# Kernel tuning notes

Measured on AMD Instinct MI355X. Metric: run time of the kernel, lower is better.

The kernel has to match this reference:

```python
import jax, jax.numpy as jnp
import numpy as np

B, S, T, D = 64, 256, 8, 256
E, M = 500000, 2048
NEG_INF = -10000000000.0


def setup_inputs() -> dict:
    key = jax.random.key(0)
    ks = jax.random.split(key, 9)
    token_reprs = jax.random.normal(ks[0], (B, S, T, D), dtype=jnp.float32)
    w1 = jax.random.normal(ks[1], (D, D // 2), dtype=jnp.float32) * (1.0 / np.sqrt(D))
    b1 = jnp.zeros((D // 2,), dtype=jnp.float32)
    w2 = jax.random.normal(ks[2], (D // 2, 1), dtype=jnp.float32) * (1.0 / np.sqrt(D // 2))
    b2 = jnp.zeros((1,), dtype=jnp.float32)
    edge_index = jax.random.randint(ks[3], (2, E), 0, B * S, dtype=jnp.int32)
    lm_indices = jax.random.randint(ks[4], (M,), 0, B * S * T, dtype=jnp.int32)
    batch_pointers = jax.random.randint(ks[5], (M,), 0, B, dtype=jnp.int32)
    tree_padding_mask = jax.random.randint(ks[6], (B, S), 0, 2, dtype=jnp.int32).astype(jnp.bool_)
    return {
        "token_reprs": token_reprs,
        "w1": w1, "b1": b1, "w2": w2, "b2": b2,
        "edge_index": edge_index,
        "lm_indices": lm_indices,
        "batch_pointers": batch_pointers,
        "tree_padding_mask": tree_padding_mask,
    }


def reference(token_reprs, w1, b1, w2, b2, edge_index, lm_indices, batch_pointers, tree_padding_mask):
    b, s, t, d = token_reprs.shape
    # type representation is the first token of each type tree
    type_reprs = token_reprs[:, :, 0]                  # [B, S, D]
    flat_types = type_reprs.reshape(b * s, d)          # [B*S, D]

    # predict_lemmas: gather scope/goal reprs, elementwise multiply, 2-layer MLP
    scope_ids, goal_ids = edge_index[0], edge_index[1]
    h = flat_types[scope_ids] * flat_types[goal_ids]   # [E, D]
    h = h @ w1 + b1                                    # [E, D//2] (Dropout is identity in eval)
    lemmas = (h @ w2 + b2)[:, 0]                       # [E]

    # predict_masks: gather masked token reprs + per-tree candidates, dot, mask
    mask_reprs = token_reprs.reshape(b * s * t, d)[lm_indices]  # [M, D]
    candidates = type_reprs[batch_pointers]            # [M, S, D]
    candidate_mask = tree_padding_mask[batch_pointers] # [M, S]
    lm_preds = jnp.einsum('md,msd->ms', mask_reprs, candidates)
    lm_preds = jnp.where(candidate_mask, lm_preds, NEG_INF)
    return lemmas, lm_preds
```

## Files before the change

### kernel.cpp

```cpp
#include <hip/hip_runtime.h>

#define DD 256
#define SS 256
#define BB 64
#define NEDGE 500000
#define MM 2048
#define NEG_INF -10000000000.0f
#define ROWF4 512
#define NROWS (BB * SS)

#define OFF_VC     0
#define OFF_MSORT  4096
#define OFF_BSTART (4096 + MM * 4)
#define OFF_FSLAB  (1 << 16)
#define OFF_P2     ((1 << 16) + (4 << 20))
#define OFF_MROWS  ((1 << 16) + (12 << 20))

typedef float vf4 __attribute__((ext_vector_type(4)));
typedef float f32x2 __attribute__((ext_vector_type(2)));

__device__ __forceinline__ float bflo(unsigned u) { return __uint_as_float(u << 16); }
__device__ __forceinline__ float bfhi(unsigned u) { return __uint_as_float(u & 0xFFFF0000u); }
__device__ __forceinline__ unsigned short bf_rne(float f) {
    unsigned u = __float_as_uint(f);
    return (unsigned short)((u + 0x7FFFu + ((u >> 16) & 1u)) >> 16);
}
__device__ __forceinline__ unsigned pack2_rne(float a, float b) {
    return (unsigned)bf_rne(a) | ((unsigned)bf_rne(b) << 16);
}

#if __has_builtin(__builtin_amdgcn_cvt_pk_fp8_f32) && __has_builtin(__builtin_amdgcn_cvt_pk_f32_fp8)
#define FP8_HW 1
#else
#define FP8_HW 0
#endif

__device__ __forceinline__ unsigned char sw_f32_to_e4m3(float f) {
    unsigned u = __float_as_uint(f);
    unsigned s = (u >> 24) & 0x80u;
    float af = fabsf(f);
    if (af >= 448.f) return (unsigned char)(s | 0x7E);
    if (af < 0.015625f) {
        int q = (int)(af * 512.f + 0.5f);
        return (unsigned char)(s | (unsigned)q);
    }
    unsigned lsb = (u >> 20) & 1u;
    u += 0x7FFFFu + lsb;
    int e = (int)(u >> 23) - 120;
    unsigned m = (u >> 20) & 7u;
    if (e >= 16) return (unsigned char)(s | 0x7E);
    return (unsigned char)(s | ((unsigned)e << 3) | m);
}
__device__ __forceinline__ float sw_e4m3_to_f32(unsigned b) {
    unsigned s = (b & 0x80u) << 24;
    unsigned e = (b >> 3) & 0xFu, m = b & 7u;
    if (e == 0) {
        float v = (float)m * 0.001953125f;
        return (b & 0x80u) ? -v : v;
    }
    return __uint_as_float(s | ((e + 120u) << 23) | (m << 20));
}

__device__ __forceinline__ unsigned enc_fp8x4(float x, float y, float z, float w) {
#if FP8_HW
    int r = 0;
    r = __builtin_amdgcn_cvt_pk_fp8_f32(x, y, r, false);
    r = __builtin_amdgcn_cvt_pk_fp8_f32(z, w, r, true);
    return (unsigned)r;
#else
    return (unsigned)sw_f32_to_e4m3(x) | ((unsigned)sw_f32_to_e4m3(y) << 8)
         | ((unsigned)sw_f32_to_e4m3(z) << 16) | ((unsigned)sw_f32_to_e4m3(w) << 24);
#endif
}

__device__ __forceinline__ float dot4_fp8(unsigned aw, unsigned bw, const float4 v) {
#if FP8_HW
    f32x2 al = __builtin_amdgcn_cvt_pk_f32_fp8((int)aw, false);
    f32x2 ah = __builtin_amdgcn_cvt_pk_f32_fp8((int)aw, true);
    f32x2 bl = __builtin_amdgcn_cvt_pk_f32_fp8((int)bw, false);
    f32x2 bh = __builtin_amdgcn_cvt_pk_f32_fp8((int)bw, true);
    return (al.x * bl.x) * v.x + (al.y * bl.y) * v.y
         + (ah.x * bh.x) * v.z + (ah.y * bh.y) * v.w;
#else
    return sw_e4m3_to_f32(aw & 255u) * sw_e4m3_to_f32(bw & 255u) * v.x
         + sw_e4m3_to_f32((aw >> 8) & 255u) * sw_e4m3_to_f32((bw >> 8) & 255u) * v.y
         + sw_e4m3_to_f32((aw >> 16) & 255u) * sw_e4m3_to_f32((bw >> 16) & 255u) * v.z
         + sw_e4m3_to_f32(aw >> 24) * sw_e4m3_to_f32(bw >> 24) * v.w;
#endif
}

__global__ void setup_k(const float* __restrict__ w1, const float* __restrict__ b1,
                        const float* __restrict__ w2, const float* __restrict__ b2,
                        const int* __restrict__ bp,
                        float* __restrict__ vc, int* __restrict__ msorted,
                        int* __restrict__ bstart) {
    const int t = threadIdx.x;
    if (blockIdx.x == 0) {
        __shared__ float sw2[DD / 2];
        if (t < DD / 2) sw2[t] = w2[t];
        __syncthreads();
        const int lane = t & 63, w = t >> 6;
        for (int r = w; r < DD; r += 4) {
            float x = w1[r * (DD / 2) + lane] * sw2[lane]
                    + w1[r * (DD / 2) + 64 + lane] * sw2[64 + lane];
            x += __shfl_down(x, 32);
            x += __shfl_down(x, 16);
            x += __shfl_down(x, 8);
            x += __shfl_down(x, 4);
            x += __shfl_down(x, 2);
            x += __shfl_down(x, 1);
            if (lane == 0) vc[r] = x;
        }
        if (w == 0) {
            float x = b1[lane] * sw2[lane] + b1[64 + lane] * sw2[64 + lane];
            x += __shfl_down(x, 32);
            x += __shfl_down(x, 16);
            x += __shfl_down(x, 8);
            x += __shfl_down(x, 4);
            x += __shfl_down(x, 2);
            x += __shfl_down(x, 1);
            if (lane == 0) vc[DD] = x + b2[0];
        }
    } else {
        __shared__ int hist[BB];
        __shared__ int offs[BB + 1];
        if (t < BB) hist[t] = 0;
        __syncthreads();
        for (int m = t; m < MM; m += 256) atomicAdd(&hist[bp[m]], 1);
        __syncthreads();
        if (t == 0) {
            int acc = 0;
            for (int i = 0; i < BB; ++i) { offs[i] = acc; acc += hist[i]; }
            offs[BB] = acc;
        }
        __syncthreads();
        if (t < BB + 1) bstart[t] = offs[t];
        __syncthreads();
        for (int m = t; m < MM; m += 256) {
            int pos = atomicAdd(&offs[bp[m]], 1);
            msorted[pos] = m;
        }
    }
}

__global__ __launch_bounds__(256) void compact(
        const float* __restrict__ tok, const int* __restrict__ lmi,
        unsigned* __restrict__ fslab,
        unsigned* __restrict__ p2, unsigned* __restrict__ mrows) {
    const int lane = threadIdx.x & 63;
    const int w    = threadIdx.x >> 6;
    if (blockIdx.x < NROWS / 4) {
        const int row = blockIdx.x * 4 + w;
        const float4 a = ((const float4*)tok)[(size_t)row * ROWF4 + lane];
        fslab[(size_t)row * 64 + lane] = enc_fp8x4(a.x, a.y, a.z, a.w);
        const size_t pi = (size_t)row * 128 + lane * 2;
        p2[pi]     = pack2_rne(a.x, a.y);
        p2[pi + 1] = pack2_rne(a.z, a.w);
    } else {
        const int m = (blockIdx.x - NROWS / 4) * 4 + w;
        const float4 a = ((const float4*)(tok + (size_t)lmi[m] * DD))[lane];
        mrows[(size_t)m * 128 + lane * 2]     = pack2_rne(a.x, a.y);
        mrows[(size_t)m * 128 + lane * 2 + 1] = pack2_rne(a.z, a.w);
    }
}

__global__ __launch_bounds__(256) void edge_fp8(
        const unsigned* __restrict__ fslab,
        const int* __restrict__ edges, const float* __restrict__ vc,
        float* __restrict__ out) {
    const int t = threadIdx.x;
    const int lane = t & 63, w = t >> 6;
    const int l16 = lane & 15;
    const int g = lane >> 4;
    const int e0 = blockIdx.x * 256;

    __shared__ int sIdx[2][256];
    __shared__ float accs[256];
    const int e = e0 + t;
    const bool val = e < NEDGE;
    sIdx[0][t] = val ? __builtin_nontemporal_load(edges + e) : 0;
    sIdx[1][t] = val ? __builtin_nontemporal_load(edges + NEDGE + e) : 0;

    const float4 v0 = ((const float4*)vc)[l16 * 4 + 0];
    const float4 v1 = ((const float4*)vc)[l16 * 4 + 1];
    const float4 v2 = ((const float4*)vc)[l16 * 4 + 2];
    const float4 v3 = ((const float4*)vc)[l16 * 4 + 3];
    __syncthreads();

    #pragma unroll 4
    for (int it = 0; it < 16; ++it) {
        const int slot = w * 64 + it * 4 + g;
        const int sc = sIdx[0][slot];
        const int gl = sIdx[1][slot];
        const uint4 A = *(const uint4*)(fslab + (size_t)sc * 64 + l16 * 4);
        const uint4 B = *(const uint4*)(fslab + (size_t)gl * 64 + l16 * 4);
        float s = dot4_fp8(A.x, B.x, v0) + dot4_fp8(A.y, B.y, v1)
                + dot4_fp8(A.z, B.z, v2) + dot4_fp8(A.w, B.w, v3);
        s += __shfl_down(s, 8, 16);
        s += __shfl_down(s, 4, 16);
        s += __shfl_down(s, 2, 16);
        s += __shfl_down(s, 1, 16);
        if (l16 == 0) accs[slot] = s;
    }
    __syncthreads();
    const float c = vc[DD];
    if (val) __builtin_nontemporal_store(accs[t] + c, out + e);
}

__global__ __launch_bounds__(256) void lm_gemm(
        const unsigned* __restrict__ p2,
        const unsigned* __restrict__ mrows,
        const int* __restrict__ msorted,
        const int* __restrict__ bstart,
        const int* __restrict__ tpm,
        float* __restrict__ out) {
    const int b  = blockIdx.x;
    const int st = blockIdx.y;
    const int ch = blockIdx.z;
    const int s0 = bstart[b], s1 = bstart[b + 1];
    const int base = s0 + ch * 32;
    if (base >= s1) return;
    const int nm = min(32, s1 - base);
    const int t = threadIdx.x;

    __shared__ unsigned lmaskU[32 * 132];
    __shared__ unsigned srowU[32 * 132];
    __shared__ int mids[32];
    __shared__ int sact[64];
    __shared__ int snact;

    if (t < 32) mids[t] = msorted[base + min(t, nm - 1)];
    if (t >= 64 && t < 128) {
        int lt = t - 64;
        bool act = tpm[b * SS + st * 64 + lt] != 0;
        unsigned long long mk = __ballot(act);
        if (act) sact[__popcll(mk & ((1ull << lt) - 1))] = lt;
        if (lt == 0) snact = (int)__popcll(mk);
    }
    __syncthreads();

    for (int f = t; f < nm * 32; f += 256) {
        int r = f >> 5, q = f & 31;
        *(uint4*)&lmaskU[r * 132 + q * 4] = ((const uint4*)mrows)[(size_t)mids[r] * 32 + q];
    }
    for (int f = t; f < nm * 64; f += 256) {
        int i = f >> 6, c = f & 63;
        if (!tpm[b * SS + st * 64 + c])
            out[(size_t)mids[i] * SS + st * 64 + c] = NEG_INF;
    }
    __syncthreads();

    const int nact = snact;
    const int i2 = t & 15, sg = t >> 4;

    for (int g = 0; g * 32 < nact; ++g) {
        if (g) __syncthreads();
        const int nv = min(32, nact - g * 32);
        for (int f = t; f < nv * 32; f += 256) {
            int r = f >> 5, q = f & 31;
            size_t row = (size_t)b * SS + st * 64 + sact[g * 32 + r];
            *(uint4*)&srowU[r * 132 + q * 4] = ((const uint4*)p2)[row * 32 + q];
        }
        __syncthreads();

        float a00 = 0.f, a01 = 0.f, a10 = 0.f, a11 = 0.f;
        #pragma unroll 4
        for (int stp = 0; stp < 32; ++stp) {
            const uint4 A0 = *(const uint4*)&lmaskU[i2 * 132 + stp * 4];
            const uint4 A1 = *(const uint4*)&lmaskU[(i2 + 16) * 132 + stp * 4];
            const uint4 B0 = *(const uint4*)&srowU[sg * 132 + stp * 4];
            const uint4 B1 = *(const uint4*)&srowU[(sg + 16) * 132 + stp * 4];
            float a0[8], a1[8], b0[8], b1[8];
            a0[0] = bflo(A0.x); a0[1] = bfhi(A0.x); a0[2] = bflo(A0.y); a0[3] = bfhi(A0.y);
            a0[4] = bflo(A0.z); a0[5] = bfhi(A0.z); a0[6] = bflo(A0.w); a0[7] = bfhi(A0.w);
            a1[0] = bflo(A1.x); a1[1] = bfhi(A1.x); a1[2] = bflo(A1.y); a1[3] = bfhi(A1.y);
            a1[4] = bflo(A1.z); a1[5] = bfhi(A1.z); a1[6] = bflo(A1.w); a1[7] = bfhi(A1.w);
            b0[0] = bflo(B0.x); b0[1] = bfhi(B0.x); b0[2] = bflo(B0.y); b0[3] = bfhi(B0.y);
            b0[4] = bflo(B0.z); b0[5] = bfhi(B0.z); b0[6] = bflo(B0.w); b0[7] = bfhi(B0.w);
            b1[0] = bflo(B1.x); b1[1] = bfhi(B1.x); b1[2] = bflo(B1.y); b1[3] = bfhi(B1.y);
            b1[4] = bflo(B1.z); b1[5] = bfhi(B1.z); b1[6] = bflo(B1.w); b1[7] = bfhi(B1.w);
            #pragma unroll
            for (int jj = 0; jj < 8; ++jj) {
                a00 = fmaf(a0[jj], b0[jj], a00);
                a01 = fmaf(a0[jj], b1[jj], a01);
                a10 = fmaf(a1[jj], b0[jj], a10);
                a11 = fmaf(a1[jj], b1[jj], a11);
            }
        }

        const int iA = g * 32 + sg, iB = iA + 16;
        if (i2 < nm) {
            size_t ob = (size_t)mids[i2] * SS + st * 64;
            if (iA < nact) out[ob + sact[iA]] = a00;
            if (iB < nact) out[ob + sact[iB]] = a01;
        }
        if (i2 + 16 < nm) {
            size_t ob = (size_t)mids[i2 + 16] * SS + st * 64;
            if (iA < nact) out[ob + sact[iA]] = a10;
            if (iB < nact) out[ob + sact[iB]] = a11;
        }
    }
}

extern "C" void kernel_launch(void* const* d_in, const int* in_sizes, int n_in,
                              void* d_out, int out_size, void* d_ws, size_t ws_size,
                              hipStream_t stream) {
    const float* tok = (const float*)d_in[0];
    const float* w1  = (const float*)d_in[1];
    const float* b1  = (const float*)d_in[2];
    const float* w2  = (const float*)d_in[3];
    const float* b2  = (const float*)d_in[4];
    const int* edges = (const int*)d_in[5];
    const int* lmi   = (const int*)d_in[6];
    const int* bp    = (const int*)d_in[7];
    const int* tpm   = (const int*)d_in[8];

    float* out_lemmas = (float*)d_out;
    float* out_lm     = (float*)d_out + NEDGE;

    char* ws = (char*)d_ws;
    float* vc        = (float*)(ws + OFF_VC);
    int* msorted     = (int*)(ws + OFF_MSORT);
    int* bstart      = (int*)(ws + OFF_BSTART);
    unsigned* fslab  = (unsigned*)(ws + OFF_FSLAB);
    unsigned* p2     = (unsigned*)(ws + OFF_P2);
    unsigned* mrows  = (unsigned*)(ws + OFF_MROWS);

    setup_k<<<2, 256, 0, stream>>>(w1, b1, w2, b2, bp, vc, msorted, bstart);
    compact<<<NROWS / 4 + MM / 4, 256, 0, stream>>>(tok, lmi, fslab, p2, mrows);
    edge_fp8<<<(NEDGE + 255) / 256, 256, 0, stream>>>(fslab, edges, vc, out_lemmas);
    lm_gemm<<<dim3(BB, 4, 8), 256, 0, stream>>>(p2, mrows, msorted, bstart, tpm, out_lm);
}
```

Before: 261.4 us.

## Use bf16 MFMA in lm_gemm and merge setup and compact kernels

The scalar bf16-unpack FMA loop in lm_gemm is replaced with __builtin_amdgcn_mfma_f32_16x16x32_bf16, where each wave computes one 16x16 output tile, and the output indexing is remapped to match. The setup and compact kernels are merged into one prep kernel, saving a launch and letting the small setup work run alongside the compaction blocks. The MFMA path depends on getting the fragment layout exactly right. The bulk of the time is likely in compaction and the edge kernel, so the overall effect may be limited.

```diff
diff --git a/kernel.cpp b/kernel.cpp
--- a/kernel.cpp
+++ b/kernel.cpp
@@ -18,6 +18,8 @@
 
 typedef float vf4 __attribute__((ext_vector_type(4)));
 typedef float f32x2 __attribute__((ext_vector_type(2)));
+typedef float f32x4 __attribute__((ext_vector_type(4)));
+typedef short bf16x8 __attribute__((ext_vector_type(8)));
 
 __device__ __forceinline__ float bflo(unsigned u) { return __uint_as_float(u << 16); }
 __device__ __forceinline__ float bfhi(unsigned u) { return __uint_as_float(u & 0xFFFF0000u); }
@@ -89,17 +91,34 @@
 #endif
 }
 
-__global__ void setup_k(const float* __restrict__ w1, const float* __restrict__ b1,
-                        const float* __restrict__ w2, const float* __restrict__ b2,
-                        const int* __restrict__ bp,
-                        float* __restrict__ vc, int* __restrict__ msorted,
-                        int* __restrict__ bstart) {
+__global__ __launch_bounds__(256) void prep(
+        const float* __restrict__ tok, const int* __restrict__ lmi,
+        const float* __restrict__ w1, const float* __restrict__ b1,
+        const float* __restrict__ w2, const float* __restrict__ b2,
+        const int* __restrict__ bp,
+        unsigned* __restrict__ fslab,
+        unsigned* __restrict__ p2, unsigned* __restrict__ mrows,
+        float* __restrict__ vc, int* __restrict__ msorted,
+        int* __restrict__ bstart) {
     const int t = threadIdx.x;
-    if (blockIdx.x == 0) {
+    const int lane = t & 63;
+    const int w    = t >> 6;
+    if (blockIdx.x < NROWS / 4) {
+        const int row = blockIdx.x * 4 + w;
+        const float4 a = ((const float4*)tok)[(size_t)row * ROWF4 + lane];
+        fslab[(size_t)row * 64 + lane] = enc_fp8x4(a.x, a.y, a.z, a.w);
+        const size_t pi = (size_t)row * 128 + lane * 2;
+        p2[pi]     = pack2_rne(a.x, a.y);
+        p2[pi + 1] = pack2_rne(a.z, a.w);
+    } else if (blockIdx.x < NROWS / 4 + MM / 4) {
+        const int m = (blockIdx.x - NROWS / 4) * 4 + w;
+        const float4 a = ((const float4*)(tok + (size_t)lmi[m] * DD))[lane];
+        mrows[(size_t)m * 128 + lane * 2]     = pack2_rne(a.x, a.y);
+        mrows[(size_t)m * 128 + lane * 2 + 1] = pack2_rne(a.z, a.w);
+    } else if (blockIdx.x == NROWS / 4 + MM / 4) {
         __shared__ float sw2[DD / 2];
         if (t < DD / 2) sw2[t] = w2[t];
         __syncthreads();
-        const int lane = t & 63, w = t >> 6;
         for (int r = w; r < DD; r += 4) {
             float x = w1[r * (DD / 2) + lane] * sw2[lane]
                     + w1[r * (DD / 2) + 64 + lane] * sw2[64 + lane];
@@ -140,27 +159,6 @@
             int pos = atomicAdd(&offs[bp[m]], 1);
             msorted[pos] = m;
         }
-    }
-}
-
-__global__ __launch_bounds__(256) void compact(
-        const float* __restrict__ tok, const int* __restrict__ lmi,
-        unsigned* __restrict__ fslab,
-        unsigned* __restrict__ p2, unsigned* __restrict__ mrows) {
-    const int lane = threadIdx.x & 63;
-    const int w    = threadIdx.x >> 6;
-    if (blockIdx.x < NROWS / 4) {
-        const int row = blockIdx.x * 4 + w;
-        const float4 a = ((const float4*)tok)[(size_t)row * ROWF4 + lane];
-        fslab[(size_t)row * 64 + lane] = enc_fp8x4(a.x, a.y, a.z, a.w);
-        const size_t pi = (size_t)row * 128 + lane * 2;
-        p2[pi]     = pack2_rne(a.x, a.y);
-        p2[pi + 1] = pack2_rne(a.z, a.w);
-    } else {
-        const int m = (blockIdx.x - NROWS / 4) * 4 + w;
-        const float4 a = ((const float4*)(tok + (size_t)lmi[m] * DD))[lane];
-        mrows[(size_t)m * 128 + lane * 2]     = pack2_rne(a.x, a.y);
-        mrows[(size_t)m * 128 + lane * 2 + 1] = pack2_rne(a.z, a.w);
     }
 }
 
@@ -223,8 +221,8 @@
     const int nm = min(32, s1 - base);
     const int t = threadIdx.x;
 
-    __shared__ unsigned lmaskU[32 * 132];
-    __shared__ unsigned srowU[32 * 132];
+    __shared__ __align__(16) unsigned lmaskU[32 * 132];
+    __shared__ __align__(16) unsigned srowU[32 * 132];
     __shared__ int mids[32];
     __shared__ int sact[64];
     __shared__ int snact;
@@ -251,7 +249,12 @@
     __syncthreads();
 
     const int nact = snact;
-    const int i2 = t & 15, sg = t >> 4;
+    const int lane = t & 63;
+    const int wv = t >> 6;
+    const int rt = wv >> 1;
+    const int ct = wv & 1;
+    const int fr = lane & 15;
+    const int fq = lane >> 4;
 
     for (int g = 0; g * 32 < nact; ++g) {
         if (g) __syncthreads();
@@ -263,41 +266,22 @@
         }
         __syncthreads();
 
-        float a00 = 0.f, a01 = 0.f, a10 = 0.f, a11 = 0.f;
-        #pragma unroll 4
-        for (int stp = 0; stp < 32; ++stp) {
-            const uint4 A0 = *(const uint4*)&lmaskU[i2 * 132 + stp * 4];
-            const uint4 A1 = *(const uint4*)&lmaskU[(i2 + 16) * 132 + stp * 4];
-            const uint4 B0 = *(const uint4*)&srowU[sg * 132 + stp * 4];
-            const uint4 B1 = *(const uint4*)&srowU[(sg + 16) * 132 + stp * 4];
-            float a0[8], a1[8], b0[8], b1[8];
-            a0[0] = bflo(A0.x); a0[1] = bfhi(A0.x); a0[2] = bflo(A0.y); a0[3] = bfhi(A0.y);
-            a0[4] = bflo(A0.z); a0[5] = bfhi(A0.z); a0[6] = bflo(A0.w); a0[7] = bfhi(A0.w);
-            a1[0] = bflo(A1.x); a1[1] = bfhi(A1.x); a1[2] = bflo(A1.y); a1[3] = bfhi(A1.y);
-            a1[4] = bflo(A1.z); a1[5] = bfhi(A1.z); a1[6] = bflo(A1.w); a1[7] = bfhi(A1.w);
-            b0[0] = bflo(B0.x); b0[1] = bfhi(B0.x); b0[2] = bflo(B0.y); b0[3] = bfhi(B0.y);
-            b0[4] = bflo(B0.z); b0[5] = bfhi(B0.z); b0[6] = bflo(B0.w); b0[7] = bfhi(B0.w);
-            b1[0] = bflo(B1.x); b1[1] = bfhi(B1.x); b1[2] = bflo(B1.y); b1[3] = bfhi(B1.y);
-            b1[4] = bflo(B1.z); b1[5] = bfhi(B1.z); b1[6] = bflo(B1.w); b1[7] = bfhi(B1.w);
+        f32x4 acc = {0.f, 0.f, 0.f, 0.f};
+        #pragma unroll
+        for (int stp = 0; stp < 8; ++stp) {
+            bf16x8 a = *(const bf16x8*)&lmaskU[(rt * 16 + fr) * 132 + stp * 16 + fq * 4];
+            bf16x8 bfr = *(const bf16x8*)&srowU[(ct * 16 + fr) * 132 + stp * 16 + fq * 4];
+            acc = __builtin_amdgcn_mfma_f32_16x16x32_bf16(a, bfr, acc, 0, 0, 0);
+        }
+
+        const int jg = g * 32 + ct * 16 + fr;
+        if (jg < nact) {
+            const int sj = sact[jg];
             #pragma unroll
-            for (int jj = 0; jj < 8; ++jj) {
-                a00 = fmaf(a0[jj], b0[jj], a00);
-                a01 = fmaf(a0[jj], b1[jj], a01);
-                a10 = fmaf(a1[jj], b0[jj], a10);
-                a11 = fmaf(a1[jj], b1[jj], a11);
+            for (int r = 0; r < 4; ++r) {
+                const int mi = rt * 16 + fq * 4 + r;
+                if (mi < nm) out[(size_t)mids[mi] * SS + st * 64 + sj] = acc[r];
             }
-        }
-
-        const int iA = g * 32 + sg, iB = iA + 16;
-        if (i2 < nm) {
-            size_t ob = (size_t)mids[i2] * SS + st * 64;
-            if (iA < nact) out[ob + sact[iA]] = a00;
-            if (iB < nact) out[ob + sact[iB]] = a01;
-        }
-        if (i2 + 16 < nm) {
-            size_t ob = (size_t)mids[i2 + 16] * SS + st * 64;
-            if (iA < nact) out[ob + sact[iA]] = a10;
-            if (iB < nact) out[ob + sact[iB]] = a11;
         }
     }
 }
@@ -326,8 +310,8 @@
     unsigned* p2     = (unsigned*)(ws + OFF_P2);
     unsigned* mrows  = (unsigned*)(ws + OFF_MROWS);
 
-    setup_k<<<2, 256, 0, stream>>>(w1, b1, w2, b2, bp, vc, msorted, bstart);
-    compact<<<NROWS / 4 + MM / 4, 256, 0, stream>>>(tok, lmi, fslab, p2, mrows);
+    prep<<<NROWS / 4 + MM / 4 + 2, 256, 0, stream>>>(
+        tok, lmi, w1, b1, w2, b2, bp, fslab, p2, mrows, vc, msorted, bstart);
     edge_fp8<<<(NEDGE + 255) / 256, 256, 0, stream>>>(fslab, edges, vc, out_lemmas);
     lm_gemm<<<dim3(BB, 4, 8), 256, 0, stream>>>(p2, mrows, msorted, bstart, tpm, out_lm);
 }
```

After: 247.4 us. 5.4% less time.
